# Optimization experiments

Measured on AMD Instinct MI355X. Metric: run time of the kernel, lower is better.

The kernel has to match this reference:

```python
import jax, jax.numpy as jnp
import numpy as np

B, T = 128, 512
V, E, H, A, L = 50000, 256, 512, 64, 2


def setup_inputs() -> dict:
    key = jax.random.key(0)
    ks = jax.random.split(key, 16)
    token_ids = jax.random.randint(ks[0], (B, T), 0, V, dtype=jnp.int32)
    # lengths must be >= 2 so that the source's (len-1)-1 index is valid
    lengths = jnp.clip(jax.random.randint(ks[1], (B,), 0, T, dtype=jnp.int32), 4, T)
    s = 0.05
    inp = {
        "token_ids": token_ids,
        "lengths": lengths,
        "embedding": jax.random.normal(ks[2], (V, E), jnp.float32) * s,
        "Wt": jax.random.normal(ks[3], (A, E), jnp.float32) * s,   # tokens_linear
        "bt": jax.random.normal(ks[4], (A,), jnp.float32) * s,
        "Wq": jax.random.normal(ks[5], (A, H), jnp.float32) * s,   # query_linear
        "bq": jax.random.normal(ks[6], (A,), jnp.float32) * s,
        "v": jax.random.normal(ks[7], (A,), jnp.float32) * s,      # attention_linear weight
        "bv": jax.random.normal(ks[8], (), jnp.float32) * s,       # attention_linear bias
        "gru_Wih0": jax.random.normal(ks[9], (3 * H, A), jnp.float32) * s,
        "gru_Whh0": jax.random.normal(ks[10], (3 * H, H), jnp.float32) * s,
        "gru_bih0": jax.random.normal(ks[11], (3 * H,), jnp.float32) * s,
        "gru_bhh0": jax.random.normal(ks[12], (3 * H,), jnp.float32) * s,
        "gru_Wih1": jax.random.normal(ks[13], (3 * H, H), jnp.float32) * s,
        "gru_Whh1": jax.random.normal(ks[14], (3 * H, H), jnp.float32) * s,
        "gru_bih1": jax.random.normal(ks[15], (3 * H,), jnp.float32) * s,
        "gru_bhh1": jax.random.normal(jax.random.fold_in(key, 99), (3 * H,), jnp.float32) * s,
    }
    return inp


def _gru_cell(x, h, Wih, Whh, bih, bhh):
    gi = x @ Wih.T + bih      # [B, 3H]
    gh = h @ Whh.T + bhh      # [B, 3H]
    i_r, i_z, i_n = jnp.split(gi, 3, axis=-1)
    h_r, h_z, h_n = jnp.split(gh, 3, axis=-1)
    r = jax.nn.sigmoid(i_r + h_r)
    z = jax.nn.sigmoid(i_z + h_z)
    n = jnp.tanh(i_n + r * h_n)
    return (1.0 - z) * n + z * h


def reference(token_ids, lengths, embedding, Wt, bt, Wq, bq, v, bv,
              gru_Wih0, gru_Whh0, gru_bih0, gru_bhh0,
              gru_Wih1, gru_Whh1, gru_bih1, gru_bhh1):
    x = embedding[token_ids]                 # [B, T, E]
    tp = jnp.einsum('bte,ae->bta', x, Wt) + bt   # tokens_linear, [B, T, A]
    pos = jnp.arange(T)

    def step(h, i):
        # query = hidden_state[-1] (zeros at step 0, matching hidden_state=None)
        q = h[-1] @ Wq.T + bq                # [B, A]
        s = jnp.tanh(tp + q[:, None, :]) @ v + bv   # [B, T]
        s = jnp.where(pos[None, :] <= i, s, -jnp.inf)  # growing prefix
        attn = jax.nn.softmax(s, axis=1)
        ctx = jnp.einsum('bt,bta->ba', attn, tp)     # [B, A]
        h0 = _gru_cell(ctx, h[0], gru_Wih0, gru_Whh0, gru_bih0, gru_bhh0)
        h1 = _gru_cell(h0, h[1], gru_Wih1, gru_Whh1, gru_bih1, gru_bhh1)
        return jnp.stack([h0, h1]), h1

    h_init = jnp.zeros((L, B, H), tp.dtype)
    _, outs = jax.lax.scan(step, h_init, jnp.arange(T))   # outs: [T, B, H]
    # source: sequence_lengths = len-1, then index sequence_lengths-1 = len-2
    idx = jnp.clip(lengths - 2, 0, T - 1)
    result = outs[idx, jnp.arange(B)]                     # [B, H]
    return result
```

## Files before the change

kernel.cpp:

```cpp
#include <hip/hip_runtime.h>

#define NB 128
#define NT 512
#define NE 256
#define NH 512
#define NA 64
#define NG 8
#define WPG 32
#define GB 16

typedef short bf16x8 __attribute__((ext_vector_type(8)));
typedef float f32x4 __attribute__((ext_vector_type(4)));
typedef unsigned short u16x8 __attribute__((ext_vector_type(8)));
typedef unsigned long long u64;

__device__ __forceinline__ unsigned short f2bf(float f){
  unsigned u = __builtin_bit_cast(unsigned, f);
  u = u + 0x7fffu + ((u >> 16) & 1u);
  return (unsigned short)(u >> 16);
}
__device__ __forceinline__ float bf2f(unsigned short h){
  unsigned u = ((unsigned)h) << 16;
  return __builtin_bit_cast(float, u);
}
__device__ __forceinline__ bf16x8 packbf2(f32x4 a, f32x4 b){
  bf16x8 r;
  r[0]=(short)f2bf(a[0]); r[1]=(short)f2bf(a[1]); r[2]=(short)f2bf(a[2]); r[3]=(short)f2bf(a[3]);
  r[4]=(short)f2bf(b[0]); r[5]=(short)f2bf(b[1]); r[6]=(short)f2bf(b[2]); r[7]=(short)f2bf(b[3]);
  return r;
}
__device__ __forceinline__ bf16x8 loadB_f32(const float* p){
  f32x4 a = *(const f32x4*)p;
  f32x4 b = *(const f32x4*)(p + 4);
  return packbf2(a, b);
}
#define MFMA(a,b,c) __builtin_amdgcn_mfma_f32_16x16x32_bf16(a,b,c,0,0,0)

__device__ __forceinline__ float fsig(float x){
  return __builtin_amdgcn_rcpf(1.f + __expf(-x));
}
__device__ __forceinline__ float ftanh(float x){
  float e2 = __expf(2.f * x);
  return 1.f - 2.f * __builtin_amdgcn_rcpf(e2 + 1.f);
}

struct fpair { float x, y; };
__device__ __forceinline__ fpair aload_f2(const float* p){
  u64 u = __hip_atomic_load((const u64*)p, __ATOMIC_RELAXED, __HIP_MEMORY_SCOPE_AGENT);
  fpair r;
  r.x = __builtin_bit_cast(float, (unsigned)u);
  r.y = __builtin_bit_cast(float, (unsigned)(u >> 32));
  return r;
}
__device__ __forceinline__ float aload_f(const float* p){
  return __hip_atomic_load(p, __ATOMIC_RELAXED, __HIP_MEMORY_SCOPE_AGENT);
}
__device__ __forceinline__ u64 astore_bf4r(unsigned short* p, f32x4 x){
  union { unsigned short s[4]; u64 u; } t;
  t.s[0]=f2bf(x[0]); t.s[1]=f2bf(x[1]); t.s[2]=f2bf(x[2]); t.s[3]=f2bf(x[3]);
  return __hip_atomic_exchange((u64*)p, t.u, __ATOMIC_RELAXED, __HIP_MEMORY_SCOPE_AGENT);
}
__device__ __forceinline__ u64 azero8r(u64* p){
  return __hip_atomic_exchange(p, 0ull, __ATOMIC_RELAXED, __HIP_MEMORY_SCOPE_AGENT);
}
__device__ __forceinline__ float afaddr(float* p, float v){
  return __hip_atomic_fetch_add(p, v, __ATOMIC_RELAXED, __HIP_MEMORY_SCOPE_AGENT);
}

__global__ __launch_bounds__(256) void k_tp(
    const int* __restrict__ tok, const float* __restrict__ emb,
    const float* __restrict__ Wt, const float* __restrict__ bt,
    unsigned short* __restrict__ tp)
{
  const int lane = threadIdx.x & 63;
  const int w = threadIdx.x >> 6;
  const int m16 = lane & 15, quad = lane >> 4;

  bf16x8 wfq[8][4];
#pragma unroll
  for (int kc = 0; kc < 8; kc++)
#pragma unroll
    for (int nt = 0; nt < 4; nt++)
      wfq[kc][nt] = loadB_f32(Wt + (nt*16 + m16)*NE + kc*32 + quad*8);

  float btv[4];
#pragma unroll
  for (int nt = 0; nt < 4; nt++) btv[nt] = bt[nt*16 + m16];

  const int gw = blockIdx.x * 4 + w;
#pragma unroll 1
  for (int it = 0; it < 4; it++){
    const int pt = gw * 4 + it;
    const int pos = pt*16 + m16;
    const long row = (long)tok[pos];
    const float* xrow = emb + row * NE;
    f32x4 acc[4] = {{0,0,0,0},{0,0,0,0},{0,0,0,0},{0,0,0,0}};
#pragma unroll
    for (int kc = 0; kc < 8; kc++){
      bf16x8 af = loadB_f32(xrow + kc*32 + quad*8);
#pragma unroll
      for (int nt = 0; nt < 4; nt++)
        acc[nt] = MFMA(af, wfq[kc][nt], acc[nt]);
    }
#pragma unroll
    for (int nt = 0; nt < 4; nt++)
#pragma unroll
      for (int r = 0; r < 4; r++){
        int posr = pt*16 + quad*4 + r;
        tp[(long)posr * NA + nt*16 + m16] = f2bf(acc[nt][r] + btv[nt]);
      }
  }
}

__global__ __launch_bounds__(256) void k_pack(
    const float* __restrict__ Wq, unsigned short* __restrict__ blob)
{
  const int lane = threadIdx.x & 63, wv = threadIdx.x >> 6;
  const int m16 = lane & 15, quad = lane >> 4;
#pragma unroll
  for (int kc = 0; kc < 16; kc++){
    bf16x8 t = loadB_f32(Wq + (long)(wv*16 + m16)*NH + kc*32 + quad*8);
    *(bf16x8*)&blob[((wv*16 + kc)*64 + lane)*8] = t;
  }
}

struct KArgs {
  const int* len;
  const float* bq; const float* v; const float* bv;
  const float* Wih0; const float* Whh0; const float* bih0; const float* bhh0;
  const float* Wih1; const float* Whh1; const float* bih1; const float* bhh1;
  const unsigned short* tp;
  const unsigned short* wqblob;
  unsigned short* h0b; unsigned short* h1b;
  float* ctxg; float* deng;
  int* ctrl;
  float* out;
};

__device__ __forceinline__ void gbar(int* cnt, int& ep){
  __syncthreads();
  ep++;
  if (threadIdx.x == 0){
    __hip_atomic_fetch_add(cnt, 1, __ATOMIC_RELAXED, __HIP_MEMORY_SCOPE_AGENT);
    const int tgt = WPG * ep;
    while (__hip_atomic_load(cnt, __ATOMIC_RELAXED, __HIP_MEMORY_SCOPE_AGENT) < tgt)
      __builtin_amdgcn_s_sleep(1);
  }
  __syncthreads();
}

__device__ __forceinline__ void stage_h(const unsigned short* hb,
                                        unsigned short (*hs)[64][8], int tid){
  const int lane = tid & 63, wv = tid >> 6;
  const int b = lane & 15, quad = lane >> 4;
#pragma unroll
  for (int c = 0; c < 4; c++){
    const int kc = wv*4 + c;
    const unsigned short* src = hb + b*NH + kc*32 + quad*8;
    union { u64 u[2]; bf16x8 v; } t;
    t.u[0] = __hip_atomic_load((const u64*)src,     __ATOMIC_RELAXED, __HIP_MEMORY_SCOPE_AGENT);
    t.u[1] = __hip_atomic_load((const u64*)(src+4), __ATOMIC_RELAXED, __HIP_MEMORY_SCOPE_AGENT);
    *(bf16x8*)&hs[kc][lane][0] = t.v;
  }
}

__global__ __launch_bounds__(256, 1) void k_main(KArgs A_)
{
  const int tid = threadIdx.x, lane = tid & 63, w = tid >> 6;
  const int g = blockIdx.x & 7, m = blockIdx.x >> 3;
  const int m16 = lane & 15, quad = lane >> 4;

  __shared__ __attribute__((aligned(16))) unsigned short h0s[16][64][8];
  __shared__ __attribute__((aligned(16))) unsigned short h1s[16][64][8];
  __shared__ __attribute__((aligned(16))) float dslab[6][256];
  __shared__ __attribute__((aligned(16))) float qs[16][68];

  unsigned short* h0b = A_.h0b + g * GB * NH;
  unsigned short* h1b = A_.h1b + g * GB * NH;
  float* ctxg = A_.ctxg + g * GB * NA;
  float* deng = A_.deng + g * GB;
  int* bar    = A_.ctrl + g * 64;
  const int b0 = g * GB;

  u64  usink = 0;
  float fsink = 0.f;

  bf16x8 wf[48], wih0f[2];
  float bhh0v[4], bih0v[4], bhh1v[4], bih1v[4];
  if (w < 3){
    const int r0 = w * NH + m * 16;
#pragma unroll
    for (int kc = 0; kc < 16; kc++){
      wf[kc]    = loadB_f32(A_.Whh0 + (long)(r0 + m16)*NH + kc*32 + quad*8);
      wf[16+kc] = loadB_f32(A_.Whh1 + (long)(r0 + m16)*NH + kc*32 + quad*8);
      wf[32+kc] = loadB_f32(A_.Wih1 + (long)(r0 + m16)*NH + kc*32 + quad*8);
    }
#pragma unroll
    for (int kc = 0; kc < 2; kc++)
      wih0f[kc] = loadB_f32(A_.Wih0 + (r0 + m16)*NA + kc*32 + quad*8);
#pragma unroll
    for (int r = 0; r < 4; r++){
      int d = r0 + quad*4 + r;
      bhh0v[r] = A_.bhh0[d]; bih0v[r] = A_.bih0[d];
      bhh1v[r] = A_.bhh1[d]; bih1v[r] = A_.bih1[d];
    }
  }
  float bqw[4];
#pragma unroll
  for (int r = 0; r < 4; r++) bqw[r] = A_.bq[w*16 + quad*4 + r];

  float vv[16];
#pragma unroll
  for (int jj = 0; jj < 16; jj++) vv[jj] = A_.v[quad*16 + jj];
  const float bvv = A_.bv[0];
  const int gwav = m*4 + w;
  const int ab = gwav & 15;
  const int wr = gwav >> 4;

  f32x4 h0p = {0,0,0,0}, h1p = {0,0,0,0};
  if (w == 3){
    f32x4 z = {0,0,0,0};
    usink += astore_bf4r(&h0b[m16*NH + m*16 + quad*4], z);
    usink += astore_bf4r(&h1b[m16*NH + m*16 + quad*4], z);
  }
  if (w == 1){
    if (lane < 16) usink += azero8r((u64*)ctxg + m*16 + lane);
    if (lane == 16 && m < 8) usink += azero8r((u64*)deng + m);
  }

  int myidx = 0, imax = 0;
#pragma unroll 1
  for (int b = 0; b < GB; b++){
    int L = A_.len[b0 + b];
    int ix = L - 2; ix = ix < 0 ? 0 : (ix > NT-1 ? NT-1 : ix);
    if (b == m16) myidx = ix;
    imax = imax > ix ? imax : ix;
  }

  int ep = 0;
  gbar(bar, ep);

  f32x4 gh0c = {0,0,0,0};
  if (w < 3){
#pragma unroll
    for (int r = 0; r < 4; r++) gh0c[r] = bhh0v[r];
  }

#pragma unroll 1
  for (int i = 0; i <= imax; i++){
    stage_h(h1b, h1s, tid);
    __syncthreads();

    f32x4 gh1 = {0,0,0,0};
    {
      f32x4 qa = {0,0,0,0};
      if (w < 3){
#pragma unroll
        for (int kc = 0; kc < 16; kc++){
          bf16x8 b1f = *(const bf16x8*)&h1s[kc][lane][0];
          gh1 = MFMA(wf[16+kc], b1f, gh1);
          bf16x8 af = *(const bf16x8*)&A_.wqblob[((w*16 + kc)*64 + lane)*8];
          qa = MFMA(af, b1f, qa);
        }
#pragma unroll
        for (int r = 0; r < 4; r++) gh1[r] += bhh1v[r];
      } else {
#pragma unroll
        for (int kc = 0; kc < 16; kc++){
          bf16x8 b1f = *(const bf16x8*)&h1s[kc][lane][0];
          bf16x8 af = *(const bf16x8*)&A_.wqblob[((w*16 + kc)*64 + lane)*8];
          qa = MFMA(af, b1f, qa);
        }
      }
#pragma unroll
      for (int r = 0; r < 4; r++)
        qs[m16][w*16 + quad*4 + r] = qa[r] + bqw[r];
    }
    __syncthreads();

    float qv[16];
#pragma unroll
    for (int jq = 0; jq < 4; jq++){
      f32x4 t = *(const f32x4*)&qs[ab][quad*16 + jq*4];
      qv[jq*4+0]=t[0]; qv[jq*4+1]=t[1]; qv[jq*4+2]=t[2]; qv[jq*4+3]=t[3];
    }
    float ctxp[16];
#pragma unroll
    for (int jj = 0; jj < 16; jj++) ctxp[jj] = 0.f;
    float denp = 0.f;
    const unsigned short* tpb = A_.tp + (long)(b0 + ab) * NT * NA;
#pragma unroll 1
    for (int c = wr; c*16 <= i; c += 8){
      const int t = c*16 + m16;
      const unsigned short* tpp = tpb + (long)t*NA + quad*16;
      u16x8 ta = *(const u16x8*)tpp;
      u16x8 tb = *(const u16x8*)(tpp + 8);
      float tpf[16];
#pragma unroll
      for (int jj = 0; jj < 8; jj++){ tpf[jj] = bf2f(ta[jj]); tpf[8+jj] = bf2f(tb[jj]); }
      float sp = 0.f;
#pragma unroll
      for (int jj = 0; jj < 16; jj++){
        float x = tpf[jj] + qv[jj];
        sp = fmaf(ftanh(x), vv[jj], sp);
      }
      sp += __shfl_xor(sp, 16);
      sp += __shfl_xor(sp, 32);
      float e = __expf(sp + bvv);
      e = (t <= i) ? e : 0.f;
      denp += e;
#pragma unroll
      for (int jj = 0; jj < 16; jj++) ctxp[jj] = fmaf(e, tpf[jj], ctxp[jj]);
    }
#pragma unroll
    for (int off = 1; off < 64; off <<= 1) denp += __shfl_xor(denp, off);
    denp *= 0.25f;
#pragma unroll
    for (int st = 0; st < 4; st++){
      const int bit = 1 << st;
      const bool up = (lane >> st) & 1;
      const int n2 = (16 >> st) >> 1;
#pragma unroll
      for (int j2 = 0; j2 < 8; j2++){
        if (j2 < n2){
          float keep = up ? ctxp[2*j2+1] : ctxp[2*j2];
          float send = up ? ctxp[2*j2]   : ctxp[2*j2+1];
          float got = __shfl_xor(send, bit);
          ctxp[j2] = keep + got;
        }
      }
    }
    fsink += afaddr(&ctxg[ab*NA + lane], ctxp[0]);
    if (lane == 0) fsink += afaddr(&deng[ab], denp);

    gbar(bar, ep);

    if (w < 3){
      f32x4 gi0 = {0,0,0,0};
      const float rdn = 1.0f / aload_f(&deng[m16]);
#pragma unroll
      for (int kc = 0; kc < 2; kc++){
        const float* cp = &ctxg[m16*NA + kc*32 + quad*8];
        f32x4 c0, c1;
        fpair p0 = aload_f2(cp+0); c0[0]=p0.x; c0[1]=p0.y;
        fpair p1 = aload_f2(cp+2); c0[2]=p1.x; c0[3]=p1.y;
        fpair p2 = aload_f2(cp+4); c1[0]=p2.x; c1[1]=p2.y;
        fpair p3 = aload_f2(cp+6); c1[2]=p3.x; c1[3]=p3.y;
#pragma unroll
        for (int r = 0; r < 4; r++){ c0[r] *= rdn; c1[r] *= rdn; }
        gi0 = MFMA(wih0f[kc], packbf2(c0, c1), gi0);
      }
#pragma unroll
      for (int r = 0; r < 4; r++) gi0[r] += bih0v[r];
      *(f32x4*)&dslab[w][lane*4] = gh0c;
      *(f32x4*)&dslab[3+w][lane*4] = gi0;
    }
    __syncthreads();
    if (w == 3){
      f32x4 ghr = *(f32x4*)&dslab[0][lane*4];
      f32x4 ghz = *(f32x4*)&dslab[1][lane*4];
      f32x4 ghn = *(f32x4*)&dslab[2][lane*4];
      f32x4 gir = *(f32x4*)&dslab[3][lane*4];
      f32x4 giz = *(f32x4*)&dslab[4][lane*4];
      f32x4 gin = *(f32x4*)&dslab[5][lane*4];
      f32x4 hn;
#pragma unroll
      for (int r = 0; r < 4; r++){
        float rr = fsig(gir[r] + ghr[r]);
        float zz = fsig(giz[r] + ghz[r]);
        float nn = ftanh(gin[r] + rr*ghn[r]);
        hn[r] = (1.f - zz)*nn + zz*h0p[r];
      }
      h0p = hn;
      usink += astore_bf4r(&h0b[m16*NH + m*16 + quad*4], hn);
    }
    gbar(bar, ep);

    stage_h(h0b, h0s, tid);
    __syncthreads();
    if (w < 3){
      f32x4 gi1 = {0,0,0,0}, g0 = {0,0,0,0};
#pragma unroll
      for (int kc = 0; kc < 16; kc++){
        bf16x8 hf = *(const bf16x8*)&h0s[kc][lane][0];
        gi1 = MFMA(wf[32+kc], hf, gi1);
        g0  = MFMA(wf[kc],    hf, g0);
      }
#pragma unroll
      for (int r = 0; r < 4; r++){ gi1[r] += bih1v[r]; g0[r] += bhh0v[r]; }
      gh0c = g0;
      *(f32x4*)&dslab[w][lane*4] = gh1;
      *(f32x4*)&dslab[3+w][lane*4] = gi1;
    }
    if (w == 1){
      if (lane < 16) usink += azero8r((u64*)ctxg + m*16 + lane);
      if (lane == 16 && m < 8) usink += azero8r((u64*)deng + m);
    }
    __syncthreads();
    if (w == 3){
      f32x4 ghr = *(f32x4*)&dslab[0][lane*4];
      f32x4 ghz = *(f32x4*)&dslab[1][lane*4];
      f32x4 ghn = *(f32x4*)&dslab[2][lane*4];
      f32x4 gir = *(f32x4*)&dslab[3][lane*4];
      f32x4 giz = *(f32x4*)&dslab[4][lane*4];
      f32x4 gin = *(f32x4*)&dslab[5][lane*4];
      f32x4 hn;
#pragma unroll
      for (int r = 0; r < 4; r++){
        float rr = fsig(gir[r] + ghr[r]);
        float zz = fsig(giz[r] + ghz[r]);
        float nn = ftanh(gin[r] + rr*ghn[r]);
        hn[r] = (1.f - zz)*nn + zz*h1p[r];
      }
      h1p = hn;
      usink += astore_bf4r(&h1b[m16*NH + m*16 + quad*4], hn);
      if (i == myidx)
        *(f32x4*)&A_.out[(long)(b0 + m16)*NH + m*16 + quad*4] = hn;
    }
    gbar(bar, ep);
  }

  u64 total = usink + (u64)__builtin_bit_cast(unsigned, fsink);
  if (total == 0x9e3779b97f4a7c15ull && A_.len[0] == -12345)
    A_.ctrl[56 + g] = (int)total;
}

extern "C" void kernel_launch(void* const* d_in, const int* in_sizes, int n_in,
                              void* d_out, int out_size, void* d_ws, size_t ws_size,
                              hipStream_t stream)
{
  (void)in_sizes; (void)n_in; (void)out_size; (void)ws_size;
  char* ws = (char*)d_ws;
  unsigned short* tp  = (unsigned short*)ws;
  unsigned short* h0b = (unsigned short*)(ws + 8388608);
  unsigned short* h1b = h0b + NB*NH;
  float* ctxg = (float*)(h1b + NB*NH);
  float* deng = ctxg + NB*NA;
  int* ctrl   = (int*)((char*)deng + 4096);
  unsigned short* wqblob = (unsigned short*)((char*)ctrl + 2048);

  (void)hipMemsetAsync(ctrl, 0, 2048, stream);

  k_tp<<<dim3(256), dim3(256), 0, stream>>>(
      (const int*)d_in[0], (const float*)d_in[2], (const float*)d_in[3],
      (const float*)d_in[4], tp);
  k_pack<<<dim3(1), dim3(256), 0, stream>>>((const float*)d_in[5], wqblob);

  KArgs ka;
  ka.len  = (const int*)d_in[1];
  ka.bq   = (const float*)d_in[6];
  ka.v    = (const float*)d_in[7];  ka.bv   = (const float*)d_in[8];
  ka.Wih0 = (const float*)d_in[9];  ka.Whh0 = (const float*)d_in[10];
  ka.bih0 = (const float*)d_in[11]; ka.bhh0 = (const float*)d_in[12];
  ka.Wih1 = (const float*)d_in[13]; ka.Whh1 = (const float*)d_in[14];
  ka.bih1 = (const float*)d_in[15]; ka.bhh1 = (const float*)d_in[16];
  ka.tp = tp; ka.wqblob = wqblob; ka.h0b = h0b; ka.h1b = h1b;
  ka.ctxg = ctxg; ka.deng = deng; ka.ctrl = ctrl; ka.out = (float*)d_out;

  k_main<<<dim3(256), dim3(256), 0, stream>>>(ka);
}
```

Before: 8.137 ms.

## Specialize waves per role and replace global barriers with counter-based flags

Waves within each block now take fixed roles: wave 0 runs the layer-0 GRU (all three gates), wave 1 runs layer 1 with Wih1 held in LDS, and waves 2-3 do the query projection and attention. The full-group barriers are replaced by per-stage arrival counters (c2/c3/c4) that waves poll, and the ctx/denominator accumulators are double-buffered by step parity so zeroing does not need an extra barrier. The intent is to cut barrier latency and let layer-1 and attention work overlap across stages. The cost is fewer waves on attention, more LDS use, and an ordering that depends on the s_waitcnt calls and relaxed atomics being correct.

```diff
diff --git a/kernel.cpp b/kernel.cpp
--- a/kernel.cpp
+++ b/kernel.cpp
@@ -13,13 +13,14 @@
 typedef float f32x4 __attribute__((ext_vector_type(4)));
 typedef unsigned short u16x8 __attribute__((ext_vector_type(8)));
 typedef unsigned long long u64;
-
-__device__ __forceinline__ unsigned short f2bf(float f){
+typedef unsigned short us;
+
+__device__ __forceinline__ us f2bf(float f){
   unsigned u = __builtin_bit_cast(unsigned, f);
   u = u + 0x7fffu + ((u >> 16) & 1u);
-  return (unsigned short)(u >> 16);
-}
-__device__ __forceinline__ float bf2f(unsigned short h){
+  return (us)(u >> 16);
+}
+__device__ __forceinline__ float bf2f(us h){
   unsigned u = ((unsigned)h) << 16;
   return __builtin_bit_cast(float, u);
 }
@@ -35,6 +36,7 @@
   return packbf2(a, b);
 }
 #define MFMA(a,b,c) __builtin_amdgcn_mfma_f32_16x16x32_bf16(a,b,c,0,0,0)
+#define WAIT_VM0() __builtin_amdgcn_s_waitcnt(0x0F70)
 
 __device__ __forceinline__ float fsig(float x){
   return __builtin_amdgcn_rcpf(1.f + __expf(-x));
@@ -55,8 +57,11 @@
 __device__ __forceinline__ float aload_f(const float* p){
   return __hip_atomic_load(p, __ATOMIC_RELAXED, __HIP_MEMORY_SCOPE_AGENT);
 }
-__device__ __forceinline__ u64 astore_bf4r(unsigned short* p, f32x4 x){
-  union { unsigned short s[4]; u64 u; } t;
+__device__ __forceinline__ int aload_i(const int* p){
+  return __hip_atomic_load(p, __ATOMIC_RELAXED, __HIP_MEMORY_SCOPE_AGENT);
+}
+__device__ __forceinline__ u64 astore_bf4r(us* p, f32x4 x){
+  union { us s[4]; u64 u; } t;
   t.s[0]=f2bf(x[0]); t.s[1]=f2bf(x[1]); t.s[2]=f2bf(x[2]); t.s[3]=f2bf(x[3]);
   return __hip_atomic_exchange((u64*)p, t.u, __ATOMIC_RELAXED, __HIP_MEMORY_SCOPE_AGENT);
 }
@@ -65,12 +70,19 @@
 }
 __device__ __forceinline__ float afaddr(float* p, float v){
   return __hip_atomic_fetch_add(p, v, __ATOMIC_RELAXED, __HIP_MEMORY_SCOPE_AGENT);
+}
+__device__ __forceinline__ void arrive(int* c){
+  if ((threadIdx.x & 63) == 0)
+    (void)__hip_atomic_fetch_add(c, 1, __ATOMIC_RELAXED, __HIP_MEMORY_SCOPE_AGENT);
+}
+__device__ __forceinline__ void pollge(int* c, int tgt){
+  while (aload_i(c) < tgt) __builtin_amdgcn_s_sleep(1);
 }
 
 __global__ __launch_bounds__(256) void k_tp(
     const int* __restrict__ tok, const float* __restrict__ emb,
     const float* __restrict__ Wt, const float* __restrict__ bt,
-    unsigned short* __restrict__ tp)
+    us* __restrict__ tp)
 {
   const int lane = threadIdx.x & 63;
   const int w = threadIdx.x >> 6;
@@ -113,7 +125,7 @@
 }
 
 __global__ __launch_bounds__(256) void k_pack(
-    const float* __restrict__ Wq, unsigned short* __restrict__ blob)
+    const float* __restrict__ Wq, us* __restrict__ blob)
 {
   const int lane = threadIdx.x & 63, wv = threadIdx.x >> 6;
   const int m16 = lane & 15, quad = lane >> 4;
@@ -129,34 +141,22 @@
   const float* bq; const float* v; const float* bv;
   const float* Wih0; const float* Whh0; const float* bih0; const float* bhh0;
   const float* Wih1; const float* Whh1; const float* bih1; const float* bhh1;
-  const unsigned short* tp;
-  const unsigned short* wqblob;
-  unsigned short* h0b; unsigned short* h1b;
-  float* ctxg; float* deng;
+  const us* tp;
+  const us* wqblob;
+  us* h0b; us* h1b;
+  float* ctxg;
+  float* deng;
   int* ctrl;
   float* out;
 };
 
-__device__ __forceinline__ void gbar(int* cnt, int& ep){
-  __syncthreads();
-  ep++;
-  if (threadIdx.x == 0){
-    __hip_atomic_fetch_add(cnt, 1, __ATOMIC_RELAXED, __HIP_MEMORY_SCOPE_AGENT);
-    const int tgt = WPG * ep;
-    while (__hip_atomic_load(cnt, __ATOMIC_RELAXED, __HIP_MEMORY_SCOPE_AGENT) < tgt)
-      __builtin_amdgcn_s_sleep(1);
-  }
-  __syncthreads();
-}
-
-__device__ __forceinline__ void stage_h(const unsigned short* hb,
-                                        unsigned short (*hs)[64][8], int tid){
+__device__ __forceinline__ void stage_h(const us* hb, us (*hs)[64][8], int tid){
   const int lane = tid & 63, wv = tid >> 6;
   const int b = lane & 15, quad = lane >> 4;
 #pragma unroll
   for (int c = 0; c < 4; c++){
     const int kc = wv*4 + c;
-    const unsigned short* src = hb + b*NH + kc*32 + quad*8;
+    const us* src = hb + b*NH + kc*32 + quad*8;
     union { u64 u[2]; bf16x8 v; } t;
     t.u[0] = __hip_atomic_load((const u64*)src,     __ATOMIC_RELAXED, __HIP_MEMORY_SCOPE_AGENT);
     t.u[1] = __hip_atomic_load((const u64*)(src+4), __ATOMIC_RELAXED, __HIP_MEMORY_SCOPE_AGENT);
@@ -169,65 +169,88 @@
   const int tid = threadIdx.x, lane = tid & 63, w = tid >> 6;
   const int g = blockIdx.x & 7, m = blockIdx.x >> 3;
   const int m16 = lane & 15, quad = lane >> 4;
-
-  __shared__ __attribute__((aligned(16))) unsigned short h0s[16][64][8];
-  __shared__ __attribute__((aligned(16))) unsigned short h1s[16][64][8];
-  __shared__ __attribute__((aligned(16))) float dslab[6][256];
+  const int d0 = m * 16;
+
+  __shared__ __attribute__((aligned(16))) us h1s[16][64][8];
+  __shared__ __attribute__((aligned(16))) us h0s[16][64][8];
+  __shared__ __attribute__((aligned(16))) us wih1s[48][64][8];
   __shared__ __attribute__((aligned(16))) float qs[16][68];
 
-  unsigned short* h0b = A_.h0b + g * GB * NH;
-  unsigned short* h1b = A_.h1b + g * GB * NH;
-  float* ctxg = A_.ctxg + g * GB * NA;
-  float* deng = A_.deng + g * GB;
-  int* bar    = A_.ctrl + g * 64;
+  us* h0b = A_.h0b + g * GB * NH;
+  us* h1b = A_.h1b + g * GB * NH;
+  float* ctxg = A_.ctxg + g * 2 * GB * NA;
+  float* deng = A_.deng + g * 2 * GB;
+  int* c2 = A_.ctrl + g * 64;
+  int* c3 = c2 + 16;
+  int* c4 = c2 + 32;
   const int b0 = g * GB;
 
-  u64  usink = 0;
-  float fsink = 0.f;
-
-  bf16x8 wf[48], wih0f[2];
-  float bhh0v[4], bih0v[4], bhh1v[4], bih1v[4];
-  if (w < 3){
-    const int r0 = w * NH + m * 16;
-#pragma unroll
-    for (int kc = 0; kc < 16; kc++){
-      wf[kc]    = loadB_f32(A_.Whh0 + (long)(r0 + m16)*NH + kc*32 + quad*8);
-      wf[16+kc] = loadB_f32(A_.Whh1 + (long)(r0 + m16)*NH + kc*32 + quad*8);
-      wf[32+kc] = loadB_f32(A_.Wih1 + (long)(r0 + m16)*NH + kc*32 + quad*8);
-    }
-#pragma unroll
-    for (int kc = 0; kc < 2; kc++)
-      wih0f[kc] = loadB_f32(A_.Wih0 + (r0 + m16)*NA + kc*32 + quad*8);
-#pragma unroll
-    for (int r = 0; r < 4; r++){
-      int d = r0 + quad*4 + r;
-      bhh0v[r] = A_.bhh0[d]; bih0v[r] = A_.bih0[d];
-      bhh1v[r] = A_.bhh1[d]; bih1v[r] = A_.bih1[d];
-    }
-  }
-  float bqw[4];
-#pragma unroll
-  for (int r = 0; r < 4; r++) bqw[r] = A_.bq[w*16 + quad*4 + r];
-
+  u64 usink = 0; float fsink = 0.f;
+
+  bf16x8 whhf[3][16];
+  bf16x8 wih0f[3][2];
+  float bh[3][4], bi[3][4];
+  if (w == 0){
+#pragma unroll
+    for (int gate = 0; gate < 3; gate++){
+#pragma unroll
+      for (int kc = 0; kc < 16; kc++)
+        whhf[gate][kc] = loadB_f32(A_.Whh0 + (long)(gate*NH + d0 + m16)*NH + kc*32 + quad*8);
+#pragma unroll
+      for (int kc = 0; kc < 2; kc++)
+        wih0f[gate][kc] = loadB_f32(A_.Wih0 + (gate*NH + d0 + m16)*NA + kc*32 + quad*8);
+#pragma unroll
+      for (int r = 0; r < 4; r++){
+        bh[gate][r] = A_.bhh0[gate*NH + d0 + quad*4 + r];
+        bi[gate][r] = A_.bih0[gate*NH + d0 + quad*4 + r];
+      }
+    }
+  } else if (w == 1){
+#pragma unroll
+    for (int gate = 0; gate < 3; gate++){
+#pragma unroll
+      for (int kc = 0; kc < 16; kc++){
+        whhf[gate][kc] = loadB_f32(A_.Whh1 + (long)(gate*NH + d0 + m16)*NH + kc*32 + quad*8);
+        *(bf16x8*)&wih1s[gate*16 + kc][lane][0] =
+            loadB_f32(A_.Wih1 + (long)(gate*NH + d0 + m16)*NH + kc*32 + quad*8);
+      }
+#pragma unroll
+      for (int r = 0; r < 4; r++){
+        bh[gate][r] = A_.bhh1[gate*NH + d0 + quad*4 + r];
+        bi[gate][r] = A_.bih1[gate*NH + d0 + quad*4 + r];
+      }
+    }
+  }
+  float bq2[2][4];
+  if (w >= 2){
+#pragma unroll
+    for (int j = 0; j < 2; j++)
+#pragma unroll
+      for (int r = 0; r < 4; r++)
+        bq2[j][r] = A_.bq[((w-2)*2 + j)*16 + quad*4 + r];
+  }
   float vv[16];
 #pragma unroll
   for (int jj = 0; jj < 16; jj++) vv[jj] = A_.v[quad*16 + jj];
   const float bvv = A_.bv[0];
-  const int gwav = m*4 + w;
-  const int ab = gwav & 15;
-  const int wr = gwav >> 4;
-
-  f32x4 h0p = {0,0,0,0}, h1p = {0,0,0,0};
-  if (w == 3){
+  const int slot = m*2 + (w - 2);
+  const int ab = slot & 15, wr = (slot >> 4) & 3;
+
+  if (w == 1){
     f32x4 z = {0,0,0,0};
-    usink += astore_bf4r(&h0b[m16*NH + m*16 + quad*4], z);
-    usink += astore_bf4r(&h1b[m16*NH + m*16 + quad*4], z);
-  }
-  if (w == 1){
-    if (lane < 16) usink += azero8r((u64*)ctxg + m*16 + lane);
-    if (lane == 16 && m < 8) usink += azero8r((u64*)deng + m);
-  }
-
+    usink += astore_bf4r(&h0b[m16*NH + d0 + quad*4], z);
+    usink += astore_bf4r(&h1b[m16*NH + d0 + quad*4], z);
+  }
+  if (w == 0){
+    if (lane < 16){
+      usink += azero8r((u64*)ctxg + m*16 + lane);
+      usink += azero8r((u64*)ctxg + 512 + m*16 + lane);
+    }
+    if (lane == 16 && m < 8){
+      usink += azero8r((u64*)deng + m);
+      usink += azero8r((u64*)deng + 8 + m);
+    }
+  }
   int myidx = 0, imax = 0;
 #pragma unroll 1
   for (int b = 0; b < GB; b++){
@@ -236,111 +259,126 @@
     if (b == m16) myidx = ix;
     imax = imax > ix ? imax : ix;
   }
-
-  int ep = 0;
-  gbar(bar, ep);
-
-  f32x4 gh0c = {0,0,0,0};
-  if (w < 3){
-#pragma unroll
-    for (int r = 0; r < 4; r++) gh0c[r] = bhh0v[r];
-  }
+  if (w < 2){
+    WAIT_VM0();
+    arrive(c4);
+  }
+  __syncthreads();
+
+  f32x4 gh0c[3];
+  if (w == 0){
+#pragma unroll
+    for (int gate = 0; gate < 3; gate++)
+#pragma unroll
+      for (int r = 0; r < 4; r++) gh0c[gate][r] = bh[gate][r];
+  }
+  f32x4 h0p = {0,0,0,0}, h1p = {0,0,0,0};
+  f32x4 gh1[3];
 
 #pragma unroll 1
   for (int i = 0; i <= imax; i++){
+    pollge(c4, 64 + 32*i);
     stage_h(h1b, h1s, tid);
     __syncthreads();
 
-    f32x4 gh1 = {0,0,0,0};
-    {
-      f32x4 qa = {0,0,0,0};
-      if (w < 3){
+    if (w >= 2){
+#pragma unroll
+      for (int j = 0; j < 2; j++){
+        const int s = (w-2)*2 + j;
+        f32x4 qa = {0,0,0,0};
 #pragma unroll
         for (int kc = 0; kc < 16; kc++){
-          bf16x8 b1f = *(const bf16x8*)&h1s[kc][lane][0];
-          gh1 = MFMA(wf[16+kc], b1f, gh1);
-          bf16x8 af = *(const bf16x8*)&A_.wqblob[((w*16 + kc)*64 + lane)*8];
-          qa = MFMA(af, b1f, qa);
+          bf16x8 af = *(const bf16x8*)&A_.wqblob[((s*16 + kc)*64 + lane)*8];
+          bf16x8 bf = *(const bf16x8*)&h1s[kc][lane][0];
+          qa = MFMA(af, bf, qa);
         }
 #pragma unroll
-        for (int r = 0; r < 4; r++) gh1[r] += bhh1v[r];
-      } else {
-#pragma unroll
-        for (int kc = 0; kc < 16; kc++){
-          bf16x8 b1f = *(const bf16x8*)&h1s[kc][lane][0];
-          bf16x8 af = *(const bf16x8*)&A_.wqblob[((w*16 + kc)*64 + lane)*8];
-          qa = MFMA(af, b1f, qa);
+        for (int r = 0; r < 4; r++)
+          qs[m16][s*16 + quad*4 + r] = qa[r] + bq2[j][r];
+      }
+    }
+    __syncthreads();
+
+    if (w == 1){
+#pragma unroll
+      for (int gate = 0; gate < 3; gate++){ f32x4 z={0,0,0,0}; gh1[gate]=z; }
+#pragma unroll
+      for (int kc = 0; kc < 16; kc++){
+        bf16x8 bf = *(const bf16x8*)&h1s[kc][lane][0];
+#pragma unroll
+        for (int gate = 0; gate < 3; gate++)
+          gh1[gate] = MFMA(whhf[gate][kc], bf, gh1[gate]);
+      }
+#pragma unroll
+      for (int gate = 0; gate < 3; gate++)
+#pragma unroll
+        for (int r = 0; r < 4; r++) gh1[gate][r] += bh[gate][r];
+    } else if (w >= 2){
+      float qv[16];
+#pragma unroll
+      for (int jq = 0; jq < 4; jq++){
+        f32x4 t = *(const f32x4*)&qs[ab][quad*16 + jq*4];
+        qv[jq*4+0]=t[0]; qv[jq*4+1]=t[1]; qv[jq*4+2]=t[2]; qv[jq*4+3]=t[3];
+      }
+      float ctxp[16];
+#pragma unroll
+      for (int jj = 0; jj < 16; jj++) ctxp[jj] = 0.f;
+      float denp = 0.f;
+      const us* tpb = A_.tp + (long)(b0 + ab) * NT * NA;
+#pragma unroll 1
+      for (int c = wr; c*16 <= i; c += 4){
+        const int t = c*16 + m16;
+        const us* tpp = tpb + (long)t*NA + quad*16;
+        u16x8 ta = *(const u16x8*)tpp;
+        u16x8 tb = *(const u16x8*)(tpp + 8);
+        float tpf[16];
+#pragma unroll
+        for (int jj = 0; jj < 8; jj++){ tpf[jj] = bf2f(ta[jj]); tpf[8+jj] = bf2f(tb[jj]); }
+        float sp = 0.f;
+#pragma unroll
+        for (int jj = 0; jj < 16; jj++){
+          float x = tpf[jj] + qv[jj];
+          sp = fmaf(ftanh(x), vv[jj], sp);
         }
-      }
-#pragma unroll
-      for (int r = 0; r < 4; r++)
-        qs[m16][w*16 + quad*4 + r] = qa[r] + bqw[r];
-    }
-    __syncthreads();
-
-    float qv[16];
-#pragma unroll
-    for (int jq = 0; jq < 4; jq++){
-      f32x4 t = *(const f32x4*)&qs[ab][quad*16 + jq*4];
-      qv[jq*4+0]=t[0]; qv[jq*4+1]=t[1]; qv[jq*4+2]=t[2]; qv[jq*4+3]=t[3];
-    }
-    float ctxp[16];
-#pragma unroll
-    for (int jj = 0; jj < 16; jj++) ctxp[jj] = 0.f;
-    float denp = 0.f;
-    const unsigned short* tpb = A_.tp + (long)(b0 + ab) * NT * NA;
-#pragma unroll 1
-    for (int c = wr; c*16 <= i; c += 8){
-      const int t = c*16 + m16;
-      const unsigned short* tpp = tpb + (long)t*NA + quad*16;
-      u16x8 ta = *(const u16x8*)tpp;
-      u16x8 tb = *(const u16x8*)(tpp + 8);
-      float tpf[16];
-#pragma unroll
-      for (int jj = 0; jj < 8; jj++){ tpf[jj] = bf2f(ta[jj]); tpf[8+jj] = bf2f(tb[jj]); }
-      float sp = 0.f;
-#pragma unroll
-      for (int jj = 0; jj < 16; jj++){
-        float x = tpf[jj] + qv[jj];
-        sp = fmaf(ftanh(x), vv[jj], sp);
-      }
-      sp += __shfl_xor(sp, 16);
-      sp += __shfl_xor(sp, 32);
-      float e = __expf(sp + bvv);
-      e = (t <= i) ? e : 0.f;
-      denp += e;
-#pragma unroll
-      for (int jj = 0; jj < 16; jj++) ctxp[jj] = fmaf(e, tpf[jj], ctxp[jj]);
-    }
-#pragma unroll
-    for (int off = 1; off < 64; off <<= 1) denp += __shfl_xor(denp, off);
-    denp *= 0.25f;
-#pragma unroll
-    for (int st = 0; st < 4; st++){
-      const int bit = 1 << st;
-      const bool up = (lane >> st) & 1;
-      const int n2 = (16 >> st) >> 1;
-#pragma unroll
-      for (int j2 = 0; j2 < 8; j2++){
-        if (j2 < n2){
-          float keep = up ? ctxp[2*j2+1] : ctxp[2*j2];
-          float send = up ? ctxp[2*j2]   : ctxp[2*j2+1];
-          float got = __shfl_xor(send, bit);
-          ctxp[j2] = keep + got;
+        sp += __shfl_xor(sp, 16);
+        sp += __shfl_xor(sp, 32);
+        float e = __expf(sp + bvv);
+        e = (t <= i) ? e : 0.f;
+        denp += e;
+#pragma unroll
+        for (int jj = 0; jj < 16; jj++) ctxp[jj] = fmaf(e, tpf[jj], ctxp[jj]);
+      }
+#pragma unroll
+      for (int off = 1; off < 64; off <<= 1) denp += __shfl_xor(denp, off);
+      denp *= 0.25f;
+#pragma unroll
+      for (int st = 0; st < 4; st++){
+        const int bit = 1 << st;
+        const bool up = (lane >> st) & 1;
+        const int n2 = (16 >> st) >> 1;
+#pragma unroll
+        for (int j2 = 0; j2 < 8; j2++){
+          if (j2 < n2){
+            float keep = up ? ctxp[2*j2+1] : ctxp[2*j2];
+            float send = up ? ctxp[2*j2]   : ctxp[2*j2+1];
+            float got = __shfl_xor(send, bit);
+            ctxp[j2] = keep + got;
+          }
         }
       }
-    }
-    fsink += afaddr(&ctxg[ab*NA + lane], ctxp[0]);
-    if (lane == 0) fsink += afaddr(&deng[ab], denp);
-
-    gbar(bar, ep);
-
-    if (w < 3){
-      f32x4 gi0 = {0,0,0,0};
-      const float rdn = 1.0f / aload_f(&deng[m16]);
+      const int par = i & 1;
+      fsink += afaddr(&ctxg[par*GB*NA + ab*NA + lane], ctxp[0]);
+      if (lane == 0) fsink += afaddr(&deng[par*GB + ab], denp);
+      WAIT_VM0();
+      arrive(c2);
+    } else {
+      pollge(c2, 64*(i+1));
+      const int par = i & 1;
+      const float rdn = 1.0f / aload_f(&deng[par*GB + m16]);
+      f32x4 gi0[3] = {{0,0,0,0},{0,0,0,0},{0,0,0,0}};
 #pragma unroll
       for (int kc = 0; kc < 2; kc++){
-        const float* cp = &ctxg[m16*NA + kc*32 + quad*8];
+        const float* cp = &ctxg[par*GB*NA + m16*NA + kc*32 + quad*8];
         f32x4 c0, c1;
         fpair p0 = aload_f2(cp+0); c0[0]=p0.x; c0[1]=p0.y;
         fpair p1 = aload_f2(cp+2); c0[2]=p1.x; c0[3]=p1.y;
@@ -348,76 +386,73 @@
         fpair p3 = aload_f2(cp+6); c1[2]=p3.x; c1[3]=p3.y;
 #pragma unroll
         for (int r = 0; r < 4; r++){ c0[r] *= rdn; c1[r] *= rdn; }
-        gi0 = MFMA(wih0f[kc], packbf2(c0, c1), gi0);
-      }
-#pragma unroll
-      for (int r = 0; r < 4; r++) gi0[r] += bih0v[r];
-      *(f32x4*)&dslab[w][lane*4] = gh0c;
-      *(f32x4*)&dslab[3+w][lane*4] = gi0;
-    }
-    __syncthreads();
-    if (w == 3){
-      f32x4 ghr = *(f32x4*)&dslab[0][lane*4];
-      f32x4 ghz = *(f32x4*)&dslab[1][lane*4];
-      f32x4 ghn = *(f32x4*)&dslab[2][lane*4];
-      f32x4 gir = *(f32x4*)&dslab[3][lane*4];
-      f32x4 giz = *(f32x4*)&dslab[4][lane*4];
-      f32x4 gin = *(f32x4*)&dslab[5][lane*4];
+        bf16x8 bfr = packbf2(c0, c1);
+#pragma unroll
+        for (int gate = 0; gate < 3; gate++)
+          gi0[gate] = MFMA(wih0f[gate][kc], bfr, gi0[gate]);
+      }
       f32x4 hn;
 #pragma unroll
       for (int r = 0; r < 4; r++){
-        float rr = fsig(gir[r] + ghr[r]);
-        float zz = fsig(giz[r] + ghz[r]);
-        float nn = ftanh(gin[r] + rr*ghn[r]);
+        float rr = fsig(gi0[0][r] + bi[0][r] + gh0c[0][r]);
+        float zz = fsig(gi0[1][r] + bi[1][r] + gh0c[1][r]);
+        float nn = ftanh(gi0[2][r] + bi[2][r] + rr*gh0c[2][r]);
         hn[r] = (1.f - zz)*nn + zz*h0p[r];
       }
       h0p = hn;
-      usink += astore_bf4r(&h0b[m16*NH + m*16 + quad*4], hn);
-    }
-    gbar(bar, ep);
-
+      usink += astore_bf4r(&h0b[m16*NH + d0 + quad*4], hn);
+      const int np = (i + 1) & 1;
+      if (lane < 16) usink += azero8r((u64*)ctxg + np*512 + m*16 + lane);
+      if (lane == 16 && m < 8) usink += azero8r((u64*)deng + np*8 + m);
+      WAIT_VM0();
+      arrive(c3);
+    }
+
+    pollge(c3, 32*(i+1));
     stage_h(h0b, h0s, tid);
     __syncthreads();
-    if (w < 3){
-      f32x4 gi1 = {0,0,0,0}, g0 = {0,0,0,0};
+
+    if (w == 1){
+      f32x4 gi1[3] = {{0,0,0,0},{0,0,0,0},{0,0,0,0}};
 #pragma unroll
       for (int kc = 0; kc < 16; kc++){
-        bf16x8 hf = *(const bf16x8*)&h0s[kc][lane][0];
-        gi1 = MFMA(wf[32+kc], hf, gi1);
-        g0  = MFMA(wf[kc],    hf, g0);
-      }
-#pragma unroll
-      for (int r = 0; r < 4; r++){ gi1[r] += bih1v[r]; g0[r] += bhh0v[r]; }
-      gh0c = g0;
-      *(f32x4*)&dslab[w][lane*4] = gh1;
-      *(f32x4*)&dslab[3+w][lane*4] = gi1;
-    }
-    if (w == 1){
-      if (lane < 16) usink += azero8r((u64*)ctxg + m*16 + lane);
-      if (lane == 16 && m < 8) usink += azero8r((u64*)deng + m);
-    }
-    __syncthreads();
-    if (w == 3){
-      f32x4 ghr = *(f32x4*)&dslab[0][lane*4];
-      f32x4 ghz = *(f32x4*)&dslab[1][lane*4];
-      f32x4 ghn = *(f32x4*)&dslab[2][lane*4];
-      f32x4 gir = *(f32x4*)&dslab[3][lane*4];
-      f32x4 giz = *(f32x4*)&dslab[4][lane*4];
-      f32x4 gin = *(f32x4*)&dslab[5][lane*4];
+        bf16x8 bf = *(const bf16x8*)&h0s[kc][lane][0];
+#pragma unroll
+        for (int gate = 0; gate < 3; gate++){
+          bf16x8 af = *(const bf16x8*)&wih1s[gate*16 + kc][lane][0];
+          gi1[gate] = MFMA(af, bf, gi1[gate]);
+        }
+      }
       f32x4 hn;
 #pragma unroll
       for (int r = 0; r < 4; r++){
-        float rr = fsig(gir[r] + ghr[r]);
-        float zz = fsig(giz[r] + ghz[r]);
-        float nn = ftanh(gin[r] + rr*ghn[r]);
+        float rr = fsig(gi1[0][r] + bi[0][r] + gh1[0][r]);
+        float zz = fsig(gi1[1][r] + bi[1][r] + gh1[1][r]);
+        float nn = ftanh(gi1[2][r] + bi[2][r] + rr*gh1[2][r]);
         hn[r] = (1.f - zz)*nn + zz*h1p[r];
       }
       h1p = hn;
-      usink += astore_bf4r(&h1b[m16*NH + m*16 + quad*4], hn);
+      usink += astore_bf4r(&h1b[m16*NH + d0 + quad*4], hn);
       if (i == myidx)
-        *(f32x4*)&A_.out[(long)(b0 + m16)*NH + m*16 + quad*4] = hn;
-    }
-    gbar(bar, ep);
+        *(f32x4*)&A_.out[(long)(b0 + m16)*NH + d0 + quad*4] = hn;
+      WAIT_VM0();
+      arrive(c4);
+    } else if (w == 0){
+      f32x4 a0={0,0,0,0}, a1={0,0,0,0}, a2={0,0,0,0};
+#pragma unroll
+      for (int kc = 0; kc < 16; kc++){
+        bf16x8 bf = *(const bf16x8*)&h0s[kc][lane][0];
+        a0 = MFMA(whhf[0][kc], bf, a0);
+        a1 = MFMA(whhf[1][kc], bf, a1);
+        a2 = MFMA(whhf[2][kc], bf, a2);
+      }
+#pragma unroll
+      for (int r = 0; r < 4; r++){
+        gh0c[0][r] = a0[r] + bh[0][r];
+        gh0c[1][r] = a1[r] + bh[1][r];
+        gh0c[2][r] = a2[r] + bh[2][r];
+      }
+    }
   }
 
   u64 total = usink + (u64)__builtin_bit_cast(unsigned, fsink);
@@ -431,13 +466,13 @@
 {
   (void)in_sizes; (void)n_in; (void)out_size; (void)ws_size;
   char* ws = (char*)d_ws;
-  unsigned short* tp  = (unsigned short*)ws;
-  unsigned short* h0b = (unsigned short*)(ws + 8388608);
-  unsigned short* h1b = h0b + NB*NH;
+  us* tp  = (us*)ws;
+  us* h0b = (us*)(ws + 8388608);
+  us* h1b = h0b + NB*NH;
   float* ctxg = (float*)(h1b + NB*NH);
-  float* deng = ctxg + NB*NA;
+  float* deng = ctxg + NG*2*GB*NA;
   int* ctrl   = (int*)((char*)deng + 4096);
-  unsigned short* wqblob = (unsigned short*)((char*)ctrl + 2048);
+  us* wqblob  = (us*)((char*)ctrl + 2048);
 
   (void)hipMemsetAsync(ctrl, 0, 2048, stream);
 
```

Result: slower. 12.38 ms (+52.2%).
